# Optimization experiments

Hardware: AMD Instinct MI355X
Metric: run time of the kernel (lower is better)

The kernel has to match this reference:

```python
import jax, jax.numpy as jnp
import numpy as np

B = 2048        # batch
D_DENSE = 13    # dense input features
F = 7           # number of sparse features
CARD = 10000    # cardinality per sparse feature (== len(tokenizer_values))
E = 64          # embedding dim per feature
D_OUT = 32      # dense arch output size
S_OUT = 32      # sparse arch output size per feature
D_HID = 2 * D_OUT   # DenseArch MLP hidden (output_size*2 per code)
S_HID = 2 * S_OUT   # SparseArch MLP hidden (output_size*2 per code)
CONCAT = D_OUT + F * S_OUT    # 256
P_IN = CONCAT * CONCAT        # 65536, flattened outer product
P_HID = 512


def setup_inputs() -> dict:
    key = jax.random.key(0)
    ks = jax.random.split(key, 18)
    s = 0.05
    return {
        "dense_features": jax.random.normal(ks[0], (B, D_DENSE), dtype=jnp.float32),
        "sparse_features": jax.random.randint(ks[1], (B, F), 0, CARD, dtype=jnp.int64),
        # tokenizer_values per feature (shared arange, as in metadata)
        "tokenizers": jnp.arange(CARD, dtype=jnp.int64),
        # embedding tables stacked over features: [F, CARD, E]
        "emb_tables": jax.random.normal(ks[2], (F, CARD, E), dtype=jnp.float32) * s,
        # DenseArch MLP
        "dw1": jax.random.normal(ks[3], (D_DENSE, D_HID), dtype=jnp.float32) * s,
        "db1": jnp.zeros((D_HID,), dtype=jnp.float32),
        "dw2": jax.random.normal(ks[4], (D_HID, D_OUT), dtype=jnp.float32) * s,
        "db2": jnp.zeros((D_OUT,), dtype=jnp.float32),
        # per-feature sparse MLPs stacked over features
        "sw1": jax.random.normal(ks[5], (F, E, S_HID), dtype=jnp.float32) * s,
        "sb1": jnp.zeros((F, S_HID), dtype=jnp.float32),
        "sw2": jax.random.normal(ks[6], (F, S_HID, S_OUT), dtype=jnp.float32) * s,
        "sb2": jnp.zeros((F, S_OUT), dtype=jnp.float32),
        # PredictionLayer MLP
        "pw1": jax.random.normal(ks[7], (P_IN, P_HID), dtype=jnp.float32) * s,
        "pb1": jnp.zeros((P_HID,), dtype=jnp.float32),
        "pw2": jax.random.normal(ks[8], (P_HID, 1), dtype=jnp.float32) * s,
        "pb2": jnp.zeros((1,), dtype=jnp.float32),
    }


def reference(dense_features, sparse_features, tokenizers, emb_tables,
              dw1, db1, dw2, db2, sw1, sb1, sw2, sb2, pw1, pb1, pw2, pb2):
    # DenseArch: MLP(13 -> 64 -> 32)
    dense_out = jnp.maximum(dense_features @ dw1 + db1, 0.0) @ dw2 + db2  # [B, D_OUT]

    # SparseArch: equality-match argmax indexing (faithful to get_indices),
    # then embedding gather and per-feature MLP, vectorized over features.
    matches = sparse_features[:, :, None] == tokenizers[None, None, :]  # [B, F, CARD]
    idx = jnp.argmax(matches, axis=2)                                   # [B, F]
    gathered = emb_tables[jnp.arange(emb_tables.shape[0])[None, :], idx]  # [B, F, E]
    h = jnp.maximum(jnp.einsum('bfe,feh->bfh', gathered, sw1) + sb1, 0.0)
    sparse_out = jnp.einsum('bfh,fho->bfo', h, sw2) + sb2                # [B, F, S_OUT]

    # DenseSparseInteractionLayer: concat -> outer product -> flatten
    concat = jnp.concatenate(
        [dense_out, sparse_out.reshape(sparse_out.shape[0], -1)], axis=1)  # [B, CONCAT]
    outer = jnp.einsum('bi,bj->bij', concat, concat)
    flattened = outer.reshape(concat.shape[0], -1)                       # [B, CONCAT^2]

    # PredictionLayer: MLP(CONCAT^2 -> P_HID -> 1) + sigmoid, squeeze
    logits = jnp.maximum(flattened @ pw1 + pb1, 0.0) @ pw2 + pb2
    return jax.nn.sigmoid(logits).squeeze()
```

## Files before the change

### kernel.cpp

```cpp
#include <hip/hip_runtime.h>
#include <hip/hip_fp16.h>
#include <math.h>

#define BATCH 2048
#define NFEAT 7
#define CARD 10000
#define CONCAT 256
#define P_HID 512

#define BM 128
#define BN 128
#define BK 64
#define KSPLIT 12
#define NUNITS 640
#define UNIT_ST (512 * 64)
#define PREP_BLOCKS (NUNITS * 2)

using f16x4   = __attribute__((ext_vector_type(4))) _Float16;
using half8   = __attribute__((ext_vector_type(8))) _Float16;
using floatx4 = __attribute__((ext_vector_type(4))) float;

__device__ __forceinline__ void dma16(const _Float16* g, _Float16* l) {
    __builtin_amdgcn_global_load_lds(
        (const __attribute__((address_space(1))) unsigned int*)g,
        (__attribute__((address_space(3))) unsigned int*)l,
        16, 0, 0);
}

__device__ __forceinline__ void unit_decode(int u, int& i, int& jw) {
    if (u < 256)      { i = u;                jw = u >> 6; }
    else if (u < 448) { int v = u - 256; i = v / 3;        jw = 1 + v % 3; }
    else if (u < 576) { int v = u - 448; i = 64 + (v >> 1); jw = 2 + (v & 1); }
    else              { i = 128 + (u - 576); jw = 3; }
}

__device__ __forceinline__ int split_t0(int ks)     { return ks * 53 + (ks < 4 ? ks : 4); }
__device__ __forceinline__ int split_ntiles(int ks) { return 53 + (ks < 4 ? 1 : 0); }

__global__ __launch_bounds__(256) void fused_pre(
    const float* __restrict__ dense, const int* __restrict__ sparse,
    const float* __restrict__ emb,
    const float* __restrict__ dw1, const float* __restrict__ db1,
    const float* __restrict__ dw2, const float* __restrict__ db2,
    const float* __restrict__ sw1, const float* __restrict__ sb1,
    const float* __restrict__ sw2, const float* __restrict__ sb2,
    const float* __restrict__ pw1,
    _Float16* __restrict__ cbf, _Float16* __restrict__ St)
{
    __shared__ __align__(16) _Float16 sh[64 * 256];
    const int tid = threadIdx.x;

    if (blockIdx.x < PREP_BLOCKS) {
        const int u = blockIdx.x >> 1, nh = blockIdx.x & 1;
        const int nb = nh * 256;
        int i, jw;
        unit_decode(u, i, jw);

#pragma unroll
        for (int m = 0; m < 16; ++m) {
            const int flat = m * 256 + tid;
            const int q = flat >> 6, c4 = flat & 63;
            const int j = (jw << 6) + q;
            floatx4 s = {0.f, 0.f, 0.f, 0.f};
            if (j >= i) {
                s = __builtin_nontemporal_load(
                    (const floatx4*)(pw1 + ((size_t)i * 256 + j) * P_HID + nb + 4 * c4));
                if (j > i) {
                    const floatx4 mv = __builtin_nontemporal_load(
                        (const floatx4*)(pw1 + ((size_t)j * 256 + i) * P_HID + nb + 4 * c4));
                    s += mv;
                }
            }
            f16x4 hv = {(_Float16)s.x, (_Float16)s.y, (_Float16)s.z, (_Float16)s.w};
            *(f16x4*)(sh + q * 256 + 4 * c4) = hv;
        }
        __syncthreads();

        const _Float16* col = sh + tid;
        _Float16* outp = St + (size_t)u * UNIT_ST + (size_t)(nb + tid) * 64;
#pragma unroll
        for (int e = 0; e < 8; ++e) {
            half8 o;
#pragma unroll
            for (int r = 0; r < 8; ++r) o[r] = col[(8 * e + r) * 256];
            *(half8*)(outp + 8 * e) = o;
        }
    } else {
        float* smem = (float*)sh;
        const int wv = tid >> 6, t = tid & 63;
        const int b = (blockIdx.x - PREP_BLOCKS) * 4 + wv;
        float* xs   = smem + wv * 13;
        float* bufA = smem + 64  + wv * 64;
        float* bufB = smem + 320 + wv * 64;

        if (t < 13) xs[t] = dense[b * 13 + t];
        __syncthreads();

        float h = db1[t];
#pragma unroll
        for (int d = 0; d < 13; ++d) h += xs[d] * dw1[d * 64 + t];
        bufA[t] = fmaxf(h, 0.f);
        __syncthreads();

        if (t < 32) {
            float o = db2[t];
#pragma unroll
            for (int k = 0; k < 64; ++k) o += bufA[k] * dw2[k * 32 + t];
            cbf[b * 256 + t] = (_Float16)o;
        }

        for (int f = 0; f < NFEAT; ++f) {
            __syncthreads();
            const int idx = sparse[b * NFEAT + f];
            bufB[t] = emb[((size_t)(f * CARD + idx)) * 64 + t];
            __syncthreads();
            float s = sb1[f * 64 + t];
#pragma unroll
            for (int e = 0; e < 64; ++e) s += bufB[e] * sw1[(f * 64 + e) * 64 + t];
            bufA[t] = fmaxf(s, 0.f);
            __syncthreads();
            if (t < 32) {
                float o = sb2[f * 32 + t];
#pragma unroll
                for (int k = 0; k < 64; ++k) o += bufA[k] * sw2[(f * 64 + k) * 32 + t];
                cbf[b * 256 + 32 + f * 32 + t] = (_Float16)o;
            }
        }
    }
}

__global__ __launch_bounds__(256, 3) void bilinear_gemm(
    const _Float16* __restrict__ cbf, const _Float16* __restrict__ St,
    _Float16* __restrict__ hidpart)
{
    __shared__ __align__(16) _Float16 Al[BM * BK];
    __shared__ _Float16 Bl[2][BN][BK];

    const int b = blockIdx.x;
    const int xcd = b & 7, slot = b >> 3;
    const int mt = slot & 15;
    const int slice = ((slot >> 4) << 3) | xcd;
    const int nt = slice & 3, ks = slice >> 2;
    const int m0 = mt * BM, n0 = nt * BN;
    const int t0 = split_t0(ks);
    const int ntiles = split_ntiles(ks);

    const int tid = threadIdx.x, lane = tid & 63, wv = tid >> 6;
    const int wrow = (wv & 1) * 64, wcol = (wv >> 1) * 64;
    const int l15 = lane & 15, l4 = lane >> 4, l7 = lane & 7;
    const int arow = tid >> 1, ajoff = (tid & 1) * 32;

    floatx4 acc[4][4];
#pragma unroll
    for (int i = 0; i < 4; ++i)
#pragma unroll
        for (int j = 0; j < 4; ++j) acc[i][j] = (floatx4){0.f, 0.f, 0.f, 0.f};

    const _Float16* crow = cbf + (m0 + arow) * 256;

    half8 pre[4][4];
#pragma unroll
    for (int jw = 0; jw < 4; ++jw)
#pragma unroll
        for (int x = 0; x < 4; ++x)
            pre[jw][x] = *(const half8*)(crow + (jw << 6) + ajoff + 8 * x);

    char* awbase = (char*)Al + arow * 128;
    const int awsz = (arow & 7) << 4;

    const int drow = wv * 32 + (lane >> 3);
    const int eswz = (lane & 7) ^ ((lane >> 3) & 7);
    const _Float16* bsrc = St + (size_t)t0 * UNIT_ST + (size_t)(n0 + drow) * 64 + eswz * 8;

    int ui_c, ujw_c;
    unit_decode(t0, ui_c, ujw_c);
    _Float16 ci_c = crow[ui_c];
#pragma unroll
    for (int p = 0; p < 4; ++p)
        dma16(bsrc + (size_t)(p * 8) * 64, &Bl[0][wv * 32 + p * 8][0]);
    bsrc += UNIT_ST;

    for (int it = 0; it < ntiles; ++it) {
        const int cur = it & 1;
        const bool more = (it + 1 < ntiles);

        if (more) {
#pragma unroll
            for (int p = 0; p < 4; ++p)
                dma16(bsrc + (size_t)(p * 8) * 64, &Bl[cur ^ 1][wv * 32 + p * 8][0]);
            bsrc += UNIT_ST;
        }

        {
            const half8 civ = {ci_c, ci_c, ci_c, ci_c, ci_c, ci_c, ci_c, ci_c};
#define AGEN(JW)                                                              \
            { *(half8*)(awbase + ((ajoff * 2 +  0) ^ awsz)) = pre[JW][0] * civ; \
              *(half8*)(awbase + ((ajoff * 2 + 16) ^ awsz)) = pre[JW][1] * civ; \
              *(half8*)(awbase + ((ajoff * 2 + 32) ^ awsz)) = pre[JW][2] * civ; \
              *(half8*)(awbase + ((ajoff * 2 + 48) ^ awsz)) = pre[JW][3] * civ; }
            switch (ujw_c) {
                case 0:  AGEN(0); break;
                case 1:  AGEN(1); break;
                case 2:  AGEN(2); break;
                default: AGEN(3); break;
            }
#undef AGEN
        }

        if (more) {
            int ui_n, ujw_n;
            unit_decode(t0 + it + 1, ui_n, ujw_n);
            ujw_c = ujw_n;
            ci_c = crow[ui_n];
        }

        if (more) asm volatile("s_waitcnt vmcnt(5) lgkmcnt(0)" ::: "memory");
        else      asm volatile("s_waitcnt vmcnt(0) lgkmcnt(0)" ::: "memory");
        __builtin_amdgcn_s_barrier();
        __builtin_amdgcn_sched_barrier(0);

        __builtin_amdgcn_s_setprio(1);
#pragma unroll
        for (int kh = 0; kh < 2; ++kh) {
            half8 af[4], bfr[4];
#pragma unroll
            for (int i = 0; i < 4; ++i) {
                const int r = wrow + i * 16 + l15;
                const int cb = (kh * 64 + l4 * 16) ^ ((r & 7) << 4);
                af[i] = *(const half8*)((const char*)Al + r * 128 + cb);
            }
            const int s = ((kh * 4 + l4) ^ l7) * 8;
#pragma unroll
            for (int j = 0; j < 4; ++j)
                bfr[j] = *(const half8*)&Bl[cur][wcol + j * 16 + l15][s];
#pragma unroll
            for (int i = 0; i < 4; ++i)
#pragma unroll
                for (int j = 0; j < 4; ++j)
                    acc[i][j] = __builtin_amdgcn_mfma_f32_16x16x32_f16(
                        af[i], bfr[j], acc[i][j], 0, 0, 0);
        }
        __builtin_amdgcn_s_setprio(0);

        __builtin_amdgcn_sched_barrier(0);
        __builtin_amdgcn_s_barrier();
    }

    _Float16* outp = hidpart + (size_t)ks * BATCH * P_HID;
    const int r0 = m0 + wrow + l4 * 4;
    const int c0 = n0 + wcol + l15;
#pragma unroll
    for (int i = 0; i < 4; ++i)
#pragma unroll
        for (int j = 0; j < 4; ++j)
#pragma unroll
            for (int r = 0; r < 4; ++r)
                outp[(size_t)(r0 + i * 16 + r) * P_HID + c0 + j * 16] =
                    (_Float16)acc[i][j][r];
}

__global__ __launch_bounds__(256) void finalize(
    const _Float16* __restrict__ hidpart,
    const float* __restrict__ pb1,
    const float* __restrict__ pw2,
    const float* __restrict__ pb2,
    float* __restrict__ out)
{
    const int b = blockIdx.x, t = threadIdx.x;
    const int wv = t >> 6, lane = t & 63;

    float acc[8];
#pragma unroll
    for (int k = 0; k < 8; ++k) acc[k] = 0.f;

#pragma unroll
    for (int si = 0; si < 3; ++si) {
        const int s = wv + 4 * si;
        const half8 v = *(const half8*)(hidpart + (size_t)s * BATCH * P_HID
                                        + (size_t)b * P_HID + lane * 8);
#pragma unroll
        for (int k = 0; k < 8; ++k) acc[k] += (float)v[k];
    }

    __shared__ float red[4 * 512];
#pragma unroll
    for (int k = 0; k < 8; ++k) red[wv * 512 + k * 64 + lane] = acc[k];
    __syncthreads();

    if (wv == 0) {
        float dot = 0.f;
#pragma unroll
        for (int k = 0; k < 8; ++k) {
            const int n = lane * 8 + k;
            float v = red[k * 64 + lane] + red[512 + k * 64 + lane]
                    + red[1024 + k * 64 + lane] + red[1536 + k * 64 + lane];
            v += pb1[n];
            v = fmaxf(v, 0.f);
            dot += v * pw2[n];
        }
#pragma unroll
        for (int off = 32; off; off >>= 1) dot += __shfl_down(dot, off, 64);
        if (lane == 0) {
            const float s = dot + pb2[0];
            out[b] = 1.f / (1.f + expf(-s));
        }
    }
}

extern "C" void kernel_launch(void* const* d_in, const int* in_sizes, int n_in,
                              void* d_out, int out_size, void* d_ws, size_t ws_size,
                              hipStream_t stream)
{
    const float* dense  = (const float*)d_in[0];
    const int*   sparse = (const int*)d_in[1];
    const float* emb = (const float*)d_in[3];
    const float* dw1 = (const float*)d_in[4];
    const float* db1 = (const float*)d_in[5];
    const float* dw2 = (const float*)d_in[6];
    const float* db2 = (const float*)d_in[7];
    const float* sw1 = (const float*)d_in[8];
    const float* sb1 = (const float*)d_in[9];
    const float* sw2 = (const float*)d_in[10];
    const float* sb2 = (const float*)d_in[11];
    const float* pw1 = (const float*)d_in[12];
    const float* pb1 = (const float*)d_in[13];
    const float* pw2 = (const float*)d_in[14];
    const float* pb2 = (const float*)d_in[15];

    char* ws = (char*)d_ws;
    _Float16* cbf     = (_Float16*)ws;
    _Float16* St      = (_Float16*)(ws + (1 << 20));
    _Float16* hidpart = (_Float16*)(ws + (1 << 20) + ((size_t)40 << 20));

    fused_pre<<<PREP_BLOCKS + BATCH / 4, 256, 0, stream>>>(
        dense, sparse, emb, dw1, db1, dw2, db2, sw1, sb1, sw2, sb2, pw1,
        cbf, St);
    bilinear_gemm<<<16 * 4 * KSPLIT, 256, 0, stream>>>(cbf, St, hidpart);
    finalize<<<BATCH, 256, 0, stream>>>(hidpart, pb1, pw2, pb2, (float*)d_out);
}
```

Before: 345.8 us.

## Double-buffer A tile, drop split-K to 8, parallelize finalize reduction

Double-buffers the generated A tile in LDS so the next unit's A is written alongside the B DMA prefetch. This leaves one barrier per iteration instead of two. Split-K is cut from 12 to 8 slices of 80 tiles each, which means fewer partial sums to write and reduce, but also fewer blocks (occupancy hint lowered to 2). The finalize kernel now spreads the final dot product across all four waves. The larger LDS footprint and the smaller grid may reduce occupancy and load balance.

```diff
diff --git a/kernel.cpp b/kernel.cpp
--- a/kernel.cpp
+++ b/kernel.cpp
@@ -11,7 +11,8 @@
 #define BM 128
 #define BN 128
 #define BK 64
-#define KSPLIT 12
+#define KSPLIT 8
+#define NTILES 80
 #define NUNITS 640
 #define UNIT_ST (512 * 64)
 #define PREP_BLOCKS (NUNITS * 2)
@@ -33,9 +34,6 @@
     else if (u < 576) { int v = u - 448; i = 64 + (v >> 1); jw = 2 + (v & 1); }
     else              { i = 128 + (u - 576); jw = 3; }
 }
-
-__device__ __forceinline__ int split_t0(int ks)     { return ks * 53 + (ks < 4 ? ks : 4); }
-__device__ __forceinline__ int split_ntiles(int ks) { return 53 + (ks < 4 ? 1 : 0); }
 
 __global__ __launch_bounds__(256) void fused_pre(
     const float* __restrict__ dense, const int* __restrict__ sparse,
@@ -129,11 +127,11 @@
     }
 }
 
-__global__ __launch_bounds__(256, 3) void bilinear_gemm(
+__global__ __launch_bounds__(256, 2) void bilinear_gemm(
     const _Float16* __restrict__ cbf, const _Float16* __restrict__ St,
     _Float16* __restrict__ hidpart)
 {
-    __shared__ __align__(16) _Float16 Al[BM * BK];
+    __shared__ __align__(16) _Float16 Al[2][BM * BK];
     __shared__ _Float16 Bl[2][BN][BK];
 
     const int b = blockIdx.x;
@@ -142,8 +140,7 @@
     const int slice = ((slot >> 4) << 3) | xcd;
     const int nt = slice & 3, ks = slice >> 2;
     const int m0 = mt * BM, n0 = nt * BN;
-    const int t0 = split_t0(ks);
-    const int ntiles = split_ntiles(ks);
+    const int t0 = ks * NTILES;
 
     const int tid = threadIdx.x, lane = tid & 63, wv = tid >> 6;
     const int wrow = (wv & 1) * 64, wcol = (wv >> 1) * 64;
@@ -165,59 +162,66 @@
         for (int x = 0; x < 4; ++x)
             pre[jw][x] = *(const half8*)(crow + (jw << 6) + ajoff + 8 * x);
 
-    char* awbase = (char*)Al + arow * 128;
     const int awsz = (arow & 7) << 4;
+
+#define AGEN(NB, JW, C)                                                        \
+    {                                                                          \
+        const half8 civ_ = {C, C, C, C, C, C, C, C};                           \
+        char* aw_ = (char*)Al[NB] + arow * 128;                                \
+        *(half8*)(aw_ + ((ajoff * 2 +  0) ^ awsz)) = pre[JW][0] * civ_;        \
+        *(half8*)(aw_ + ((ajoff * 2 + 16) ^ awsz)) = pre[JW][1] * civ_;        \
+        *(half8*)(aw_ + ((ajoff * 2 + 32) ^ awsz)) = pre[JW][2] * civ_;        \
+        *(half8*)(aw_ + ((ajoff * 2 + 48) ^ awsz)) = pre[JW][3] * civ_;        \
+    }
+#define AGEN_SW(NB, JW, C)                                                     \
+    switch (JW) {                                                              \
+        case 0:  AGEN(NB, 0, C); break;                                        \
+        case 1:  AGEN(NB, 1, C); break;                                        \
+        case 2:  AGEN(NB, 2, C); break;                                        \
+        default: AGEN(NB, 3, C); break;                                        \
+    }
 
     const int drow = wv * 32 + (lane >> 3);
     const int eswz = (lane & 7) ^ ((lane >> 3) & 7);
     const _Float16* bsrc = St + (size_t)t0 * UNIT_ST + (size_t)(n0 + drow) * 64 + eswz * 8;
 
-    int ui_c, ujw_c;
-    unit_decode(t0, ui_c, ujw_c);
-    _Float16 ci_c = crow[ui_c];
-#pragma unroll
-    for (int p = 0; p < 4; ++p)
-        dma16(bsrc + (size_t)(p * 8) * 64, &Bl[0][wv * 32 + p * 8][0]);
-    bsrc += UNIT_ST;
-
-    for (int it = 0; it < ntiles; ++it) {
+    {
+        int ui0, ujw0; unit_decode(t0, ui0, ujw0);
+        const _Float16 ci0 = crow[ui0];
+#pragma unroll
+        for (int p = 0; p < 4; ++p)
+            dma16(bsrc + (size_t)(p * 8) * 64, &Bl[0][wv * 32 + p * 8][0]);
+        bsrc += UNIT_ST;
+        AGEN_SW(0, ujw0, ci0);
+    }
+    int ujw_n;
+    _Float16 ci_n;
+    {
+        int ui1, j1; unit_decode(t0 + 1, ui1, j1);
+        ujw_n = j1;
+        ci_n = crow[ui1];
+    }
+    asm volatile("s_waitcnt vmcnt(1) lgkmcnt(0)" ::: "memory");
+    __builtin_amdgcn_s_barrier();
+    __builtin_amdgcn_sched_barrier(0);
+
+    for (int it = 0; it < NTILES; ++it) {
         const int cur = it & 1;
-        const bool more = (it + 1 < ntiles);
-
-        if (more) {
+        const bool more1 = (it + 1 < NTILES);
+        const bool more2 = (it + 2 < NTILES);
+
+        if (more1) {
 #pragma unroll
             for (int p = 0; p < 4; ++p)
                 dma16(bsrc + (size_t)(p * 8) * 64, &Bl[cur ^ 1][wv * 32 + p * 8][0]);
             bsrc += UNIT_ST;
-        }
-
-        {
-            const half8 civ = {ci_c, ci_c, ci_c, ci_c, ci_c, ci_c, ci_c, ci_c};
-#define AGEN(JW)                                                              \
-            { *(half8*)(awbase + ((ajoff * 2 +  0) ^ awsz)) = pre[JW][0] * civ; \
-              *(half8*)(awbase + ((ajoff * 2 + 16) ^ awsz)) = pre[JW][1] * civ; \
-              *(half8*)(awbase + ((ajoff * 2 + 32) ^ awsz)) = pre[JW][2] * civ; \
-              *(half8*)(awbase + ((ajoff * 2 + 48) ^ awsz)) = pre[JW][3] * civ; }
-            switch (ujw_c) {
-                case 0:  AGEN(0); break;
-                case 1:  AGEN(1); break;
-                case 2:  AGEN(2); break;
-                default: AGEN(3); break;
-            }
-#undef AGEN
-        }
-
-        if (more) {
-            int ui_n, ujw_n;
-            unit_decode(t0 + it + 1, ui_n, ujw_n);
-            ujw_c = ujw_n;
-            ci_c = crow[ui_n];
-        }
-
-        if (more) asm volatile("s_waitcnt vmcnt(5) lgkmcnt(0)" ::: "memory");
-        else      asm volatile("s_waitcnt vmcnt(0) lgkmcnt(0)" ::: "memory");
-        __builtin_amdgcn_s_barrier();
-        __builtin_amdgcn_sched_barrier(0);
+            AGEN_SW(cur ^ 1, ujw_n, ci_n);
+        }
+        if (more2) {
+            int ui2, j2; unit_decode(t0 + it + 2, ui2, j2);
+            ujw_n = j2;
+            ci_n = crow[ui2];
+        }
 
         __builtin_amdgcn_s_setprio(1);
 #pragma unroll
@@ -227,7 +231,7 @@
             for (int i = 0; i < 4; ++i) {
                 const int r = wrow + i * 16 + l15;
                 const int cb = (kh * 64 + l4 * 16) ^ ((r & 7) << 4);
-                af[i] = *(const half8*)((const char*)Al + r * 128 + cb);
+                af[i] = *(const half8*)((const char*)Al[cur] + r * 128 + cb);
             }
             const int s = ((kh * 4 + l4) ^ l7) * 8;
 #pragma unroll
@@ -242,9 +246,17 @@
         }
         __builtin_amdgcn_s_setprio(0);
 
-        __builtin_amdgcn_sched_barrier(0);
-        __builtin_amdgcn_s_barrier();
-    }
+        if (more1) {
+            if (more2)
+                asm volatile("s_waitcnt vmcnt(1) lgkmcnt(0)" ::: "memory");
+            else
+                asm volatile("s_waitcnt vmcnt(0) lgkmcnt(0)" ::: "memory");
+            __builtin_amdgcn_s_barrier();
+            __builtin_amdgcn_sched_barrier(0);
+        }
+    }
+#undef AGEN_SW
+#undef AGEN
 
     _Float16* outp = hidpart + (size_t)ks * BATCH * P_HID;
     const int r0 = m0 + wrow + l4 * 4;
@@ -274,7 +286,7 @@
     for (int k = 0; k < 8; ++k) acc[k] = 0.f;
 
 #pragma unroll
-    for (int si = 0; si < 3; ++si) {
+    for (int si = 0; si < 2; ++si) {
         const int s = wv + 4 * si;
         const half8 v = *(const half8*)(hidpart + (size_t)s * BATCH * P_HID
                                         + (size_t)b * P_HID + lane * 8);
@@ -287,23 +299,26 @@
     for (int k = 0; k < 8; ++k) red[wv * 512 + k * 64 + lane] = acc[k];
     __syncthreads();
 
-    if (wv == 0) {
-        float dot = 0.f;
-#pragma unroll
-        for (int k = 0; k < 8; ++k) {
-            const int n = lane * 8 + k;
-            float v = red[k * 64 + lane] + red[512 + k * 64 + lane]
-                    + red[1024 + k * 64 + lane] + red[1536 + k * 64 + lane];
-            v += pb1[n];
-            v = fmaxf(v, 0.f);
-            dot += v * pw2[n];
-        }
-#pragma unroll
-        for (int off = 32; off; off >>= 1) dot += __shfl_down(dot, off, 64);
-        if (lane == 0) {
-            const float s = dot + pb2[0];
-            out[b] = 1.f / (1.f + expf(-s));
-        }
+    float dotw = 0.f;
+#pragma unroll
+    for (int kk = 0; kk < 2; ++kk) {
+        const int k = wv * 2 + kk;
+        const int n = lane * 8 + k;
+        float v = red[k * 64 + lane] + red[512 + k * 64 + lane]
+                + red[1024 + k * 64 + lane] + red[1536 + k * 64 + lane];
+        v += pb1[n];
+        v = fmaxf(v, 0.f);
+        dotw += v * pw2[n];
+    }
+#pragma unroll
+    for (int off = 32; off; off >>= 1) dotw += __shfl_down(dotw, off, 64);
+
+    __shared__ float r2[4];
+    if (lane == 0) r2[wv] = dotw;
+    __syncthreads();
+    if (t == 0) {
+        const float s = r2[0] + r2[1] + r2[2] + r2[3] + pb2[0];
+        out[b] = 1.f / (1.f + expf(-s));
     }
 }
 
```

New measurement: 352.3 us. About the same (+1.9%).
